# Kernel optimization log

Measured on AMD Instinct MI355X. Metric: run time of the kernel, lower is better.

Reference implementation:

```python
import jax, jax.numpy as jnp
import numpy as np
from math import factorial, sqrt

MAX_RADIUS = 5.0
NUM_BASIS = 10
N_ATOMS = 200_000
N_EDGES = 3_200_000
N_GRAPHS = 2000

# ---- real-basis Clebsch-Gordan (l x l -> l) coefficients, computed once ----

def _cg(j1, m1, j2, m2, j3, m3):
    if m1 + m2 != m3:
        return 0.0
    f = factorial
    pre = sqrt((2*j3+1) * f(j3+j1-j2) * f(j3-j1+j2) * f(j1+j2-j3) / f(j1+j2+j3+1))
    pre *= sqrt(f(j3+m3)*f(j3-m3)*f(j1-m1)*f(j1+m1)*f(j2-m2)*f(j2+m2))
    s = 0.0
    kmin = max(0, j2-j3-m1, j1-j3+m2)
    kmax = min(j1+j2-j3, j1-m1, j2+m2)
    for k in range(kmin, kmax+1):
        s += (-1)**k / (f(k)*f(j1+j2-j3-k)*f(j1-m1-k)*f(j2+m2-k)*f(j3-j2+m1+k)*f(j3-j1-m2+k))
    return pre * s

def _U_real(l):
    U = np.zeros((2*l+1, 2*l+1), dtype=np.complex128)
    U[l, l] = 1.0
    for m in range(1, l+1):
        U[l+m, l+m] = (-1)**m / sqrt(2)
        U[l+m, l-m] = 1.0 / sqrt(2)
        U[l-m, l-m] = 1j / sqrt(2)
        U[l-m, l+m] = -1j * (-1)**m / sqrt(2)
    return U

def _real_cg(l):
    n = 2*l+1
    Cc = np.zeros((n, n, n), dtype=np.complex128)
    for m1 in range(-l, l+1):
        for m2 in range(-l, l+1):
            for m3 in range(-l, l+1):
                Cc[m1+l, m2+l, m3+l] = _cg(l, m1, l, m2, l, m3)
    U = _U_real(l)
    Cr = np.einsum('ai,bj,ck,ijk->abc', U, U, U.conj(), Cc)
    if np.abs(Cr.imag).max() > np.abs(Cr.real).max():
        Cr = Cr / 1j
    Cr = Cr.real
    return Cr / np.linalg.norm(Cr)

_C1 = jnp.asarray(_real_cg(1), dtype=jnp.float32)  # [3,3,3]
_C2 = jnp.asarray(_real_cg(2), dtype=jnp.float32)  # [5,5,5]


def _edge_embedding(r):
    # soft_one_hot_linspace, basis='smooth_finite', cutoff=True
    values = jnp.linspace(0.0, MAX_RADIUS, NUM_BASIS + 2)[1:-1]
    step = MAX_RADIUS / (NUM_BASIS + 1)
    d = (r[:, None] - values) / step          # [E, NUM_BASIS]
    inside = jnp.abs(d) < 1.0
    denom = jnp.where(inside, 1.0 - d * d, 1.0)
    bump = 1.14136 * jnp.exp(2.0 - 2.0 / denom)
    return jnp.where(inside, bump, 0.0) * jnp.sqrt(float(NUM_BASIS))


def setup_inputs() -> dict:
    key = jax.random.key(0)
    ks = jax.random.split(key, 10)
    inp = {
        'H_s': jax.random.normal(ks[0], (N_ATOMS, 4), jnp.float32),
        'H_p': jax.random.normal(ks[1], (N_ATOMS, 3, 3, 3), jnp.float32),
        'H_d': jax.random.normal(ks[2], (N_ATOMS, 2, 5, 5), jnp.float32),
        'pos': jax.random.normal(ks[3], (N_ATOMS, 3), jnp.float32) * 2.0,
        'w_s': jax.random.normal(ks[4], (1,), jnp.float32),
        'w_p': jax.random.normal(ks[5], (1,), jnp.float32),
        'w_d': jax.random.normal(ks[6], (1,), jnp.float32),
        'edge_src': jax.random.randint(ks[7], (N_EDGES,), 0, N_ATOMS, jnp.int32),
        'edge_dst': jax.random.randint(ks[8], (N_EDGES,), 0, N_ATOMS, jnp.int32),
        'graph_ids': jax.random.randint(ks[9], (N_ATOMS,), 0, N_GRAPHS, jnp.int32),
        'num_graphs': N_GRAPHS,
    }
    return inp


def reference(H_s, H_p, H_d, pos, w_s, w_p, w_d, edge_src, edge_dst, graph_ids, num_graphs):
    N = H_s.shape[0]
    n_s, n_p, n_d = H_s.shape[1], H_p.shape[1], H_d.shape[1]

    # s channel: sequential 0e x 0e -> 0e tensor products == scalar product chain
    ts = jnp.prod(w_s[0] * H_s, axis=1)               # [N]
    s_feat = (ts * ts / float(n_s * n_s))[:, None]    # [N,1] gram / n_s^2

    def channel(C, Hblk, w, dim, n):
        # tensor_X = eye(dim); for each shell block: TP_l(tensor_X, H_block)
        t0 = jnp.broadcast_to(jnp.eye(dim, dtype=Hblk.dtype), (N, dim, dim))
        scale = w[0] * jnp.sqrt(float(dim))           # sqrt(2l+1) path norm
        def step(t, Hb):                              # t,Hb: [N,dim,dim]
            return scale * jnp.einsum('ijk,nbi,nbj->nbk', C, t, Hb), None
        t, _ = jax.lax.scan(step, t0, jnp.moveaxis(Hblk, 1, 0))
        gram = jnp.einsum('nbk,nck->nbc', t, t) / float(n * n)
        return gram.reshape(N, dim * dim)

    p_feat = channel(_C1, H_p, w_p, 3, n_p)           # [N,9]
    d_feat = channel(_C2, H_d, w_d, 5, n_d)           # [N,25]

    minimal_basis = jnp.concatenate([s_feat, p_feat, d_feat], axis=1)  # [N,35]

    edge_vec = pos[edge_dst] - pos[edge_src]          # [E,3]
    r = jnp.sqrt(jnp.sum(edge_vec * edge_vec, axis=1) + 1e-12)
    emb = _edge_embedding(r)                          # [E,NUM_BASIS]

    out = jax.ops.segment_sum(minimal_basis.sum(axis=1), graph_ids, num_segments=num_graphs)
    return out, emb
```

## Files before the change

kernel.cpp:

```cpp
#include <hip/hip_runtime.h>
#include <cstddef>

typedef float floatx4 __attribute__((ext_vector_type(4)));

#define K_A 0.2390457218668787f
#define K_B 0.11952286093343936f
#define K_G 0.20701966780270626f

struct C2T {
    float v[5][5][5];
    constexpr C2T() : v{} {
        v[2][2][2] = -K_A;
        v[2][1][1] = -K_B; v[2][3][3] = -K_B; v[1][2][1] = -K_B;
        v[3][2][3] = -K_B; v[1][1][2] = -K_B; v[3][3][2] = -K_B;
        v[2][0][0] =  K_A; v[2][4][4] =  K_A; v[0][2][0] =  K_A;
        v[4][2][4] =  K_A; v[0][0][2] =  K_A; v[4][4][2] =  K_A;
        v[1][1][4] =  K_G; v[4][1][1] =  K_G; v[1][4][1] =  K_G;
        v[3][3][4] = -K_G; v[4][3][3] = -K_G; v[3][4][3] = -K_G;
        v[1][3][0] = -K_G; v[3][1][0] = -K_G; v[0][1][3] = -K_G;
        v[0][3][1] = -K_G; v[1][0][3] = -K_G; v[3][0][1] = -K_G;
    }
};
constexpr C2T C2c{};

__global__ __launch_bounds__(256) void zero_kernel(float* __restrict__ out, int n) {
    int i = blockIdx.x * blockDim.x + threadIdx.x;
    if (i < n) out[i] = 0.0f;
}

__global__ __launch_bounds__(256) void pos4_kernel(
    const float* __restrict__ pos, float4* __restrict__ pos4, int N)
{
    int i = blockIdx.x * blockDim.x + threadIdx.x;
    if (i < N)
        pos4[i] = make_float4(pos[3*i], pos[3*i+1], pos[3*i+2], 0.0f);
}

__global__ __launch_bounds__(256) void atom_kernel(
    const float* __restrict__ Hs, const float* __restrict__ Hp,
    const float* __restrict__ Hd, const int* __restrict__ gid,
    const float* __restrict__ wsp, const float* __restrict__ wpp,
    const float* __restrict__ wdp, float* __restrict__ out, int N)
{
    int n = blockIdx.x * blockDim.x + threadIdx.x;
    if (n >= N) return;
    const float ws = wsp[0], wp = wpp[0], wd = wdp[0];

    const float4 hs = *(const float4*)(Hs + (size_t)n * 4);
    const float ws2 = ws * ws;
    const float ts = (ws2 * ws2) * hs.x * hs.y * hs.z * hs.w;
    float total = ts * ts * (1.0f / 16.0f);

    {
        const float* hp = Hp + (size_t)n * 27;
        const float cp = -wp * 0.70710678118654752f;
        float t[3][3] = {{1,0,0},{0,1,0},{0,0,1}};
        #pragma unroll
        for (int s = 0; s < 3; s++) {
            #pragma unroll
            for (int b = 0; b < 3; b++) {
                const float h0 = hp[s*9 + b*3 + 0];
                const float h1 = hp[s*9 + b*3 + 1];
                const float h2 = hp[s*9 + b*3 + 2];
                const float c0 = t[b][1]*h2 - t[b][2]*h1;
                const float c1 = t[b][2]*h0 - t[b][0]*h2;
                const float c2 = t[b][0]*h1 - t[b][1]*h0;
                t[b][0] = cp * c0; t[b][1] = cp * c1; t[b][2] = cp * c2;
            }
        }
        const float u0 = t[0][0] + t[1][0] + t[2][0];
        const float u1 = t[0][1] + t[1][1] + t[2][1];
        const float u2 = t[0][2] + t[1][2] + t[2][2];
        total += (u0*u0 + u1*u1 + u2*u2) * (1.0f / 9.0f);
    }

    {
        const float* hd = Hd + (size_t)n * 50;
        const float sd = wd * 2.23606797749978969f;
        float u[5] = {0, 0, 0, 0, 0};
        #pragma unroll
        for (int b = 0; b < 5; b++) {
            float h0r[5], h1r[5], t1r[5];
            #pragma unroll
            for (int j = 0; j < 5; j++) h0r[j] = hd[b*5 + j];
            #pragma unroll
            for (int k = 0; k < 5; k++) {
                float acc = 0.0f;
                #pragma unroll
                for (int j = 0; j < 5; j++) acc += C2c.v[b][j][k] * h0r[j];
                t1r[k] = sd * acc;
            }
            #pragma unroll
            for (int j = 0; j < 5; j++) h1r[j] = hd[25 + b*5 + j];
            #pragma unroll
            for (int k = 0; k < 5; k++) {
                float acc = 0.0f;
                #pragma unroll
                for (int i = 0; i < 5; i++)
                    #pragma unroll
                    for (int j = 0; j < 5; j++)
                        acc += C2c.v[i][j][k] * (t1r[i] * h1r[j]);
                u[k] += sd * acc;
            }
        }
        total += (u[0]*u[0] + u[1]*u[1] + u[2]*u[2] + u[3]*u[3] + u[4]*u[4]) * 0.25f;
    }

    unsafeAtomicAdd(out + gid[n], total);
}

__device__ __forceinline__ float bumpf(float d) {
    const float SC = 1.14136f * 3.16227766016838f;
    const float denom = 1.0f - d * d;
    const float inv = __builtin_amdgcn_rcpf(denom);
    return SC * __expf(2.0f - 2.0f * inv);
}

template <int USE4>
__global__ __launch_bounds__(256) void edge_kernel(
    const void* __restrict__ posv, const int* __restrict__ src,
    const int* __restrict__ dst, float* __restrict__ emb, int E)
{
    __shared__ float lds[256 * 11];
    const int tid  = threadIdx.x;
    const int base = blockIdx.x * 256;
    const int nb   = min(256, E - base);
    const int e    = base + tid;

    if (tid < nb) {
        const int s = __builtin_nontemporal_load(src + e);
        const int d = __builtin_nontemporal_load(dst + e);
        float dx, dy, dz;
        if (USE4) {
            const floatx4* p4 = (const floatx4*)posv;
            const floatx4 a = p4[s];
            const floatx4 b = p4[d];
            dx = b.x - a.x; dy = b.y - a.y; dz = b.z - a.z;
        } else {
            const float* p = (const float*)posv;
            dx = p[d*3+0] - p[s*3+0];
            dy = p[d*3+1] - p[s*3+1];
            dz = p[d*3+2] - p[s*3+2];
        }
        const float r  = sqrtf(dx*dx + dy*dy + dz*dz + 1e-12f);
        const float rs = r * 2.2f;
        const float fq = floorf(rs);
        const int   qa = (int)fq;
        const float va = bumpf(rs - fq);
        const float vb = bumpf(rs - fq - 1.0f);
        #pragma unroll
        for (int q = 0; q < 10; q++) {
            float v = 0.0f;
            v = (qa == q + 1) ? va : v;
            v = (qa == q)     ? vb : v;
            lds[tid * 11 + q] = v;
        }
    }
    __syncthreads();

    float* outp = emb + (size_t)base * 10;
    if (nb == 256) {
        #pragma unroll
        for (int it = 0; it < 3; it++) {
            const int t4 = tid + it * 256;
            if (t4 < 640) {
                const int j = t4 * 4;
                floatx4 v;
                v.x = lds[((j+0)/10)*11 + (j+0)%10];
                v.y = lds[((j+1)/10)*11 + (j+1)%10];
                v.z = lds[((j+2)/10)*11 + (j+2)%10];
                v.w = lds[((j+3)/10)*11 + (j+3)%10];
                __builtin_nontemporal_store(v, (floatx4*)outp + t4);
            }
        }
    } else {
        const int tot = nb * 10;
        for (int k = tid; k < tot; k += 256)
            outp[k] = lds[(k/10)*11 + k%10];
    }
}

extern "C" void kernel_launch(void* const* d_in, const int* in_sizes, int n_in,
                              void* d_out, int out_size, void* d_ws, size_t ws_size,
                              hipStream_t stream) {
    const float* Hs  = (const float*)d_in[0];
    const float* Hp  = (const float*)d_in[1];
    const float* Hd  = (const float*)d_in[2];
    const float* pos = (const float*)d_in[3];
    const float* wsp = (const float*)d_in[4];
    const float* wpp = (const float*)d_in[5];
    const float* wdp = (const float*)d_in[6];
    const int* esrc  = (const int*)d_in[7];
    const int* edst  = (const int*)d_in[8];
    const int* gid   = (const int*)d_in[9];

    const int N = in_sizes[0] / 4;
    const int E = in_sizes[7];
    const int G = out_size - 10 * E;

    float* out = (float*)d_out;
    float* emb = out + G;

    zero_kernel<<<(G + 255) / 256, 256, 0, stream>>>(out, G);

    const bool use4 = ws_size >= (size_t)N * sizeof(float4);
    if (use4) {
        float4* pos4 = (float4*)d_ws;
        pos4_kernel<<<(N + 255) / 256, 256, 0, stream>>>(pos, pos4, N);
        atom_kernel<<<(N + 255) / 256, 256, 0, stream>>>(Hs, Hp, Hd, gid, wsp, wpp, wdp, out, N);
        edge_kernel<1><<<(E + 255) / 256, 256, 0, stream>>>(pos4, esrc, edst, emb, E);
    } else {
        atom_kernel<<<(N + 255) / 256, 256, 0, stream>>>(Hs, Hp, Hd, gid, wsp, wpp, wdp, out, N);
        edge_kernel<0><<<(E + 255) / 256, 256, 0, stream>>>(pos, esrc, edst, emb, E);
    }
}
```

Before: 113.6 us.

## Stash padded float4 positions in output tail and merge zeroing launch

```diff
diff --git a/kernel.cpp b/kernel.cpp
--- a/kernel.cpp
+++ b/kernel.cpp
@@ -23,17 +23,17 @@
 };
 constexpr C2T C2c{};
 
-__global__ __launch_bounds__(256) void zero_kernel(float* __restrict__ out, int n) {
-    int i = blockIdx.x * blockDim.x + threadIdx.x;
-    if (i < n) out[i] = 0.0f;
-}
-
-__global__ __launch_bounds__(256) void pos4_kernel(
-    const float* __restrict__ pos, float4* __restrict__ pos4, int N)
+__global__ __launch_bounds__(256) void pos4zero_kernel(
+    const float* __restrict__ pos, float* __restrict__ stash,
+    float* __restrict__ out, int N, int G)
 {
     int i = blockIdx.x * blockDim.x + threadIdx.x;
-    if (i < N)
-        pos4[i] = make_float4(pos[3*i], pos[3*i+1], pos[3*i+2], 0.0f);
+    if (i < G) out[i] = 0.0f;
+    if (i < N) {
+        floatx4 v;
+        v.x = pos[3*i]; v.y = pos[3*i+1]; v.z = pos[3*i+2]; v.w = 0.0f;
+        *((floatx4*)stash + i) = v;
+    }
 }
 
 __global__ __launch_bounds__(256) void atom_kernel(
@@ -119,12 +119,13 @@
 template <int USE4>
 __global__ __launch_bounds__(256) void edge_kernel(
     const void* __restrict__ posv, const int* __restrict__ src,
-    const int* __restrict__ dst, float* __restrict__ emb, int E)
+    const int* __restrict__ dst, float* __restrict__ emb,
+    int e_begin, int e_end)
 {
     __shared__ float lds[256 * 11];
     const int tid  = threadIdx.x;
-    const int base = blockIdx.x * 256;
-    const int nb   = min(256, E - base);
+    const int base = e_begin + blockIdx.x * 256;
+    const int nb   = min(256, e_end - base);
     const int e    = base + tid;
 
     if (tid < nb) {
@@ -201,16 +202,23 @@
     float* out = (float*)d_out;
     float* emb = out + G;
 
-    zero_kernel<<<(G + 255) / 256, 256, 0, stream>>>(out, G);
-
-    const bool use4 = ws_size >= (size_t)N * sizeof(float4);
-    if (use4) {
-        float4* pos4 = (float4*)d_ws;
-        pos4_kernel<<<(N + 255) / 256, 256, 0, stream>>>(pos, pos4, N);
+    int stash_abs = (out_size - 4 * N) & ~3;
+    int Esplit = (stash_abs - G) / 10;
+    if (Esplit > E) Esplit = E;
+
+    if (Esplit > 0 && stash_abs > G) {
+        float* stash = out + stash_abs;
+        const int T0 = (N > G ? N : G);
+        pos4zero_kernel<<<(T0 + 255) / 256, 256, 0, stream>>>(pos, stash, out, N, G);
         atom_kernel<<<(N + 255) / 256, 256, 0, stream>>>(Hs, Hp, Hd, gid, wsp, wpp, wdp, out, N);
-        edge_kernel<1><<<(E + 255) / 256, 256, 0, stream>>>(pos4, esrc, edst, emb, E);
+        edge_kernel<1><<<(Esplit + 255) / 256, 256, 0, stream>>>(stash, esrc, edst, emb, 0, Esplit);
+        if (E > Esplit) {
+            const int nB = E - Esplit;
+            edge_kernel<0><<<(nB + 255) / 256, 256, 0, stream>>>(pos, esrc, edst, emb, Esplit, E);
+        }
     } else {
+        pos4zero_kernel<<<(G + 255) / 256, 256, 0, stream>>>(pos, out, out, 0, G);
         atom_kernel<<<(N + 255) / 256, 256, 0, stream>>>(Hs, Hp, Hd, gid, wsp, wpp, wdp, out, N);
-        edge_kernel<0><<<(E + 255) / 256, 256, 0, stream>>>(pos, esrc, edst, emb, E);
-    }
-}
+        edge_kernel<0><<<(E + 255) / 256, 256, 0, stream>>>(pos, esrc, edst, emb, 0, E);
+    }
+}
```

Measured after the change: 115.0 us. Within noise of the previous version (+1.2%).
